# Performance work log

Hardware: AMD Instinct MI355X
Metric: run time of the kernel (lower is better)

## Reference

```python
import jax, jax.numpy as jnp
import numpy as np

N_NODES = 200000
E = 100000
H = 128            # hidden_dim = memory_dim = time_dim
EF = 64            # edge_feat_dim (raw_msg_dim)
L = 50             # price_seq_dim
LH = 32            # LSTM hidden size
MSG_DIM = EF + 2 * H + H  # IdentityMessage output = 448
N_PARTIES, N_STATES = 8, 56


def setup_inputs() -> dict:
    key = jax.random.key(0)
    ks = jax.random.split(key, 32)
    f = lambda k, shp, s=0.05: jax.random.normal(k, shp, dtype=jnp.float32) * s
    return {
        "src": jax.random.randint(ks[0], (E,), 0, N_NODES),
        "dst": jax.random.randint(ks[1], (E,), 0, N_NODES),
        "t": jnp.sort(jax.random.randint(ks[2], (E,), 0, 1000000)),
        "msg": jax.random.normal(ks[3], (E, EF), dtype=jnp.float32),
        "price_seq": jax.random.normal(ks[4], (E, L), dtype=jnp.float32),
        "trade_t": jax.random.randint(ks[5], (E,), 0, 1000000),
        "x_static": jax.random.randint(ks[6], (N_NODES, 2), 0, N_PARTIES),
        # TGN memory state
        "memory": f(ks[7], (N_NODES, H), 0.1),
        "last_update": jax.random.uniform(ks[8], (N_NODES,), dtype=jnp.float32) * 1000.0,
        # time encoder: cos(Linear(dt))
        "w_t": f(ks[9], (H,), 0.01),
        "b_t": f(ks[10], (H,)),
        # GRUCell memory updater
        "W_ih": f(ks[11], (3 * H, MSG_DIM)),
        "b_ih": f(ks[12], (3 * H,)),
        "W_hh": f(ks[13], (3 * H, H)),
        "b_hh": f(ks[14], (3 * H,)),
        # static embeddings + projection
        "party_emb": f(ks[15], (N_PARTIES, 16), 1.0),
        "state_emb": f(ks[16], (N_STATES, 16), 1.0),
        "W_sp": f(ks[17], (H, 32)),
        "b_sp": f(ks[18], (H,)),
        # price LSTM (input_size=1, hidden=32)
        "W_ih_l": f(ks[19], (4 * LH, 1)),
        "W_hh_l": f(ks[20], (4 * LH, LH)),
        "b_ih_l": f(ks[21], (4 * LH,)),
        "b_hh_l": f(ks[22], (4 * LH,)),
        "W_pp": f(ks[23], (H, LH)),
        "b_pp": f(ks[24], (H,)),
        # predictor MLP (dropout inactive at inference)
        "W1": f(ks[25], (64, 3 * H)),
        "b1": f(ks[26], (64,)),
        "W2": f(ks[27], (1, 64)),
        "b2": f(ks[28], (1,)),
    }


def reference(src, dst, t, msg, price_seq, trade_t, x_static, memory, last_update,
              w_t, b_t, W_ih, b_ih, W_hh, b_hh, party_emb, state_emb, W_sp, b_sp,
              W_ih_l, W_hh_l, b_ih_l, b_hh_l, W_pp, b_pp, W1, b1, W2, b2):
    N, Hd = memory.shape
    tf = t.astype(jnp.float32)
    t_enc = lambda dt: jnp.cos(dt[:, None] * w_t[None, :] + b_t[None, :])

    # ---- TGNMemory.update_state: gather -> message -> last-aggregate -> GRU scatter ----
    mem_s, mem_d = memory[src], memory[dst]
    msg_s = jnp.concatenate([mem_s, mem_d, msg, t_enc(tf - last_update[src])], axis=-1)
    msg_d = jnp.concatenate([mem_d, mem_s, msg, t_enc(tf - last_update[dst])], axis=-1)
    msgs = jnp.concatenate([msg_s, msg_d], axis=0)        # [2E, MSG_DIM]
    idx = jnp.concatenate([src, dst])                     # [2E]
    te = jnp.concatenate([tf, tf])
    M = idx.shape[0]
    # LastAggregator: per node, keep the message with the largest t (ties -> later event)
    perm = jnp.argsort(te)                                # stable ascending
    ranks = jnp.zeros((M,), jnp.int32).at[perm].set(jnp.arange(M, dtype=jnp.int32))
    win_rank = jax.ops.segment_max(ranks, idx, num_segments=N)  # int32 min for empty segs
    has_msg = win_rank >= 0
    win = perm[jnp.clip(win_rank, 0, M - 1)]
    agg = jnp.where(has_msg[:, None], msgs[win], 0.0)     # [N, MSG_DIM]
    # GRUCell update (applied only to nodes with messages)
    gi = agg @ W_ih.T + b_ih
    gh = memory @ W_hh.T + b_hh
    ir, iz, inn = jnp.split(gi, 3, axis=-1)
    hr, hz, hn = jnp.split(gh, 3, axis=-1)
    r = jax.nn.sigmoid(ir + hr)
    z = jax.nn.sigmoid(iz + hz)
    n = jnp.tanh(inn + r * hn)
    mem_new = jnp.where(has_msg[:, None], (1.0 - z) * n + z * memory, memory)

    # ---- static embeddings ----
    sf = jnp.concatenate([party_emb[x_static[src, 0]], state_emb[x_static[src, 1]]], axis=1)
    src_static = sf @ W_sp.T + b_sp

    # ---- price LSTM (input_size=1) ----
    B = price_seq.shape[0]
    nLH = W_hh_l.shape[1]
    bias = b_ih_l + b_hh_l

    def step(carry, x_t):
        h, c = carry
        g = x_t[:, None] * W_ih_l[:, 0][None, :] + h @ W_hh_l.T + bias
        i, fg, gg, o = jnp.split(g, 4, axis=-1)
        c = jax.nn.sigmoid(fg) * c + jax.nn.sigmoid(i) * jnp.tanh(gg)
        h = jax.nn.sigmoid(o) * jnp.tanh(c)
        return (h, c), None

    h0 = jnp.zeros((B, nLH), price_seq.dtype)
    (h_n, _), _ = jax.lax.scan(step, (h0, h0), price_seq.T)
    price_emb = h_n @ W_pp.T + b_pp

    # ---- fuse contexts + predictor MLP (dropout = identity at eval) ----
    combined = jnp.concatenate([mem_new[src] + src_static,
                                mem_new[dst] + price_emb,
                                price_emb], axis=1)
    h1 = jax.nn.relu(combined @ W1.T + b1)
    return (h1 @ W2.T + b2)[:, 0]
```

## Files before the change

kernel.cpp:

```cpp
#include <hip/hip_runtime.h>
#include <stdint.h>

#define NN    200000
#define NE    100000
#define HD    128
#define EFD   64
#define NG    384

typedef unsigned long long u64;
typedef short bf16x8 __attribute__((ext_vector_type(8)));
typedef float f32x4  __attribute__((ext_vector_type(4)));

#define OFF_KEY   ((size_t)0)
#define OFF_CNT   ((size_t)1600000)
#define OFF_LIST  ((size_t)1600256)
#define OFF_UV    ((size_t)2400256)
#define OFF_HN    ((size_t)104800256)
#define OFF_A     ((size_t)117600256)
#define OFF_B     ((size_t)117608448)
#define OFF_C0    ((size_t)117616640)
#define OFF_WBF   ((size_t)117616896)
#define WS_NEED   ((size_t)118092032)

#define W1OFF 221184
#define GRUB  3128
#define LSTB  782

__device__ __forceinline__ float frcp(float x){ return __builtin_amdgcn_rcpf(x); }
__device__ __forceinline__ float sigf(float x){ return frcp(1.f + __expf(-x)); }
__device__ __forceinline__ float tanhf_(float x){ return 1.f - 2.f*frcp(__expf(2.f*x) + 1.f); }
__device__ __forceinline__ float4 ld4(const float* p){ return *reinterpret_cast<const float4*>(p); }

__device__ __forceinline__ short f2bf(float f){
  unsigned u = __float_as_uint(f);
  u += 0x7fffu + ((u>>16)&1u);
  return (short)(u>>16);
}
__device__ __forceinline__ unsigned cvtpk(float lo, float hi){
  unsigned r;
  asm("v_cvt_pk_bf16_f32 %0, %1, %2" : "=v"(r) : "v"(lo), "v"(hi));
  return r;
}
__device__ __forceinline__ void gl16(const void* g, void* l) {
  __builtin_amdgcn_global_load_lds(
      (const __attribute__((address_space(1))) void*)g,
      (__attribute__((address_space(3))) void*)l, 16, 0, 0);
}

__global__ void k_scatter(const int* __restrict__ src, const int* __restrict__ dst,
                          const int* __restrict__ t, u64* __restrict__ key) {
  int e = blockIdx.x*256 + threadIdx.x;
  if (e >= NE) return;
  u64 tt = (u64)(unsigned)(t[e] + 1);
  atomicMax(&key[src[e]], (tt<<18) | (u64)(unsigned)e);
  atomicMax(&key[dst[e]], (tt<<18) | (1ULL<<17) | (u64)(unsigned)e);
}

__global__ void k_compact(const u64* __restrict__ key, int* __restrict__ list,
                          int* __restrict__ count) {
  int n = blockIdx.x*256 + threadIdx.x;
  if (n >= NN) return;
  if (key[n] != 0ULL) { int p = atomicAdd(count, 1); list[p] = n; }
}

__global__ void k_pre(const float* __restrict__ W1, const float* __restrict__ W_sp,
                      const float* __restrict__ W_pp, const float* __restrict__ b_sp,
                      const float* __restrict__ b_pp, const float* __restrict__ b1,
                      float* __restrict__ A, float* __restrict__ B, float* __restrict__ c0)
{
  int tid = blockIdx.x*256 + threadIdx.x;
  if (tid < 2048) {
    int o = tid >> 5, j = tid & 31;
    float s = 0.f;
    for (int k = 0; k < 128; ++k) s = fmaf(W1[o*NG + k], W_sp[k*32 + j], s);
    A[tid] = s;
  } else if (tid < 4096) {
    int q = tid - 2048;
    int o = q >> 5, j = q & 31;
    float s = 0.f;
    for (int k = 0; k < 128; ++k)
      s = fmaf(W1[o*NG + 128 + k] + W1[o*NG + 256 + k], W_pp[k*32 + j], s);
    B[q] = s;
  } else if (tid < 4160) {
    int o = tid - 4096;
    float s = b1[o];
    for (int k = 0; k < 128; ++k) {
      s = fmaf(W1[o*NG + k], b_sp[k], s);
      s = fmaf(W1[o*NG + 128 + k] + W1[o*NG + 256 + k], b_pp[k], s);
    }
    c0[o] = s;
  }
}

__global__ void k_prew(const float* __restrict__ W_ih, const float* __restrict__ W_hh,
                       const float* __restrict__ W1, short* __restrict__ Wbf)
{
  int idx = blockIdx.x*256 + threadIdx.x;
  if (idx < 9*384*8) {
    int s   = idx & 7;
    int n   = (idx >> 3) % 384;
    int ch9 = idx / (384*8);
    int k8  = s ^ (n & 7);
    int k   = ch9*64 + k8*8;
    short v[8];
    #pragma unroll
    for (int e = 0; e < 8; ++e) {
      int kk = k + e;
      float f = (kk < 448) ? W_ih[(size_t)n*448 + kk] : W_hh[(size_t)n*HD + (kk-448)];
      v[e] = f2bf(f);
    }
    *reinterpret_cast<bf16x8*>(Wbf + (size_t)ch9*24576 + n*64 + s*8) =
        *reinterpret_cast<bf16x8*>(v);
  } else if (idx < 9*384*8 + 128*16) {
    int idx2 = idx - 9*384*8;
    int s = idx2 & 15, r = idx2 >> 4;
    int k8 = s ^ (r & 15);
    int k = k8*8;
    short v[8];
    #pragma unroll
    for (int e = 0; e < 8; ++e) {
      int kk = k + e;
      float f = (r < 64) ? W1[(size_t)r*NG + kk] : W1[(size_t)(r-64)*NG + 128 + kk];
      v[e] = f2bf(f);
    }
    *reinterpret_cast<bf16x8*>(Wbf + W1OFF + r*128 + s*8) =
        *reinterpret_cast<bf16x8*>(v);
  }
}

__global__ __launch_bounds__(512, 2) void k_gl(
    const u64* __restrict__ key, const int* __restrict__ list, const int* __restrict__ count,
    const int* __restrict__ src, const int* __restrict__ dst, const int* __restrict__ t,
    const float* __restrict__ msg, const float* __restrict__ memory,
    const float* __restrict__ last_update,
    const float* __restrict__ w_t, const float* __restrict__ b_t,
    const short* __restrict__ Wbf, const float* __restrict__ b_ih,
    const float* __restrict__ b_hh, float* __restrict__ uv,
    const float* __restrict__ price, const float* __restrict__ W_ihl,
    const float* __restrict__ W_hhl, const float* __restrict__ b_ihl,
    const float* __restrict__ b_hhl, float* __restrict__ hn_out)
{
  __shared__ char lds[60416];
  int bid = blockIdx.x;
  int tid = threadIdx.x;
  int wid = tid >> 6, lane = tid & 63;
  int lr = lane & 15, lk = lane >> 4;

  if (bid >= LSTB) {
    int g = bid - LSTB;
    short* Wsb   = reinterpret_cast<short*>(lds);
    short* Xsb   = reinterpret_cast<short*>(lds + 49152);
    float* bias4 = reinterpret_cast<float*>(lds + 57344);
    int*   sn_self  = reinterpret_cast<int*>(lds + 59392);
    int*   sn_other = reinterpret_cast<int*>(lds + 59648);
    int*   sn_e     = reinterpret_cast<int*>(lds + 59904);
    float* sn_dt    = reinterpret_cast<float*>(lds + 60160);
    short* Mn2 = &Wsb[16384];

    int cnt = count[0];
    int base = g * 64;
    if (base >= cnt) return;

    if (tid < 64) {
      int idx = base + tid;
      int cl = idx < cnt ? idx : (cnt - 1);
      int n = list[cl];
      u64 k = key[n];
      int e   = (int)(k & 0x1FFFFULL);
      int isd = (int)((k >> 17) & 1ULL);
      sn_self[tid]  = n;
      sn_other[tid] = isd ? src[e] : dst[e];
      sn_e[tid]     = e;
      sn_dt[tid]    = (float)t[e] - last_update[n];
    }
    if (tid < 128) {
      int h = tid;
      bias4[h]       = b_ih[h]       + b_hh[h];
      bias4[128 + h] = b_ih[128 + h] + b_hh[128 + h];
      bias4[256 + h] = b_ih[256 + h];
      bias4[384 + h] = b_hh[256 + h];
    }
    __syncthreads();

    f32x4 aR[4], aZ[4], aNX[4], aNM[4];
    #pragma unroll
    for (int mt = 0; mt < 4; ++mt) { aR[mt] = (f32x4)0.f; aZ[mt] = (f32x4)0.f;
                                     aNX[mt] = (f32x4)0.f; aNM[mt] = (f32x4)0.f; }

    int node8 = tid >> 3, k8s = tid & 7;

    float4 xA0, xB0, xA1, xB1, xA2, xB2, xA3, xB3, xA4, xB4;
    {
      const float* pSelf  = memory + (size_t)sn_self[node8]*HD  + k8s*8;
      const float* pOther = memory + (size_t)sn_other[node8]*HD + k8s*8;
      const float* pMsg   = msg + (size_t)sn_e[node8]*EFD + k8s*8;
      xA0 = ld4(pSelf);       xB0 = ld4(pSelf+4);
      xA1 = ld4(pSelf+64);    xB1 = ld4(pSelf+68);
      xA2 = ld4(pOther);      xB2 = ld4(pOther+4);
      xA3 = ld4(pOther+64);   xB3 = ld4(pOther+68);
      xA4 = ld4(pMsg);        xB4 = ld4(pMsg+4);
    }

    constexpr int WCH[9] = {0, 7, 1, 8, 2, 3, 4, 5, 6};
    constexpr int XST[9] = {0,-1, 1,-1, 2, 3, 4,-2,-2};

    int hrow = wid*16 + lr;
    int swzH = (hrow & 7);

    #pragma unroll
    for (int p = 0; p < 9; ++p) {
      const int W = WCH[p];
      #pragma unroll
      for (int i = 0; i < 6; ++i) {
        int q = i*512 + tid;
        gl16(Wbf + (size_t)W*24576 + q*8, &Wsb[q*8]);
      }
      if (XST[p] >= 0) {
        float4 fa, fb;
        switch (XST[p]) {
          case 0: fa = xA0; fb = xB0; break;
          case 1: fa = xA1; fb = xB1; break;
          case 2: fa = xA2; fb = xB2; break;
          case 3: fa = xA3; fb = xB3; break;
          default: fa = xA4; fb = xB4; break;
        }
        short xs[8];
        xs[0]=f2bf(fa.x); xs[1]=f2bf(fa.y); xs[2]=f2bf(fa.z); xs[3]=f2bf(fa.w);
        xs[4]=f2bf(fb.x); xs[5]=f2bf(fb.y); xs[6]=f2bf(fb.z); xs[7]=f2bf(fb.w);
        *reinterpret_cast<bf16x8*>(&Xsb[node8*64 + ((k8s ^ (node8&7))<<3)]) =
            *reinterpret_cast<bf16x8*>(xs);
      } else if (XST[p] == -2) {
        int kk = (W == 6 ? 64 : 0) + k8s*8;
        float dt = sn_dt[node8];
        short xs[8];
        #pragma unroll
        for (int q = 0; q < 8; ++q) xs[q] = f2bf(cosf(fmaf(dt, w_t[kk+q], b_t[kk+q])));
        *reinterpret_cast<bf16x8*>(&Xsb[node8*64 + ((k8s ^ (node8&7))<<3)]) =
            *reinterpret_cast<bf16x8*>(xs);
      }
      __syncthreads();

      #pragma unroll
      for (int ks = 0; ks < 2; ++ks) {
        int k8 = ks*4 + lk;
        int so = (k8 ^ swzH) << 3;
        bf16x8 bR = *reinterpret_cast<const bf16x8*>(&Wsb[(size_t)hrow*64 + so]);
        bf16x8 bZ = *reinterpret_cast<const bf16x8*>(&Wsb[(size_t)(128+hrow)*64 + so]);
        bf16x8 bN = *reinterpret_cast<const bf16x8*>(&Wsb[(size_t)(256+hrow)*64 + so]);
        #pragma unroll
        for (int mt = 0; mt < 4; ++mt) {
          int anode = mt*16 + lr;
          bf16x8 a = *reinterpret_cast<const bf16x8*>(&Xsb[anode*64 + ((k8 ^ (anode&7))<<3)]);
          aR[mt] = __builtin_amdgcn_mfma_f32_16x16x32_bf16(a, bR, aR[mt], 0, 0, 0);
          aZ[mt] = __builtin_amdgcn_mfma_f32_16x16x32_bf16(a, bZ, aZ[mt], 0, 0, 0);
          if (W < 7) aNX[mt] = __builtin_amdgcn_mfma_f32_16x16x32_bf16(a, bN, aNX[mt], 0, 0, 0);
          else       aNM[mt] = __builtin_amdgcn_mfma_f32_16x16x32_bf16(a, bN, aNM[mt], 0, 0, 0);
        }
      }
      __syncthreads();
    }

    #pragma unroll
    for (int i = 0; i < 4; ++i) {
      int q = i*512 + tid;
      gl16(Wbf + W1OFF + q*8, &Wsb[q*8]);
    }

    {
      int h = hrow;
      int k8h = h >> 3, eh = h & 7;
      float br_ = bias4[h], bz_ = bias4[128+h], bnx_ = bias4[256+h], bnm_ = bias4[384+h];
      #pragma unroll
      for (int mt = 0; mt < 4; ++mt) {
        #pragma unroll
        for (int i = 0; i < 4; ++i) {
          int node = mt*16 + lk*4 + i;
          float r  = sigf(aR[mt][i] + br_);
          float z  = sigf(aZ[mt][i] + bz_);
          float nv = tanhf_(aNX[mt][i] + bnx_ + r*(aNM[mt][i] + bnm_));
          float m  = memory[(size_t)sn_self[node]*HD + h];
          Mn2[node*128 + ((k8h ^ (node&15))<<3) + eh] = f2bf((1.f - z)*nv + z*m);
        }
      }
    }
    __syncthreads();

    {
      int orow = wid*16 + lr;
      f32x4 acc2[4];
      #pragma unroll
      for (int mt = 0; mt < 4; ++mt) acc2[mt] = (f32x4)0.f;
      #pragma unroll
      for (int kf = 0; kf < 4; ++kf) {
        int k8 = kf*4 + lk;
        bf16x8 b = *reinterpret_cast<const bf16x8*>(&Wsb[orow*128 + ((k8 ^ (orow&15))<<3)]);
        #pragma unroll
        for (int mt = 0; mt < 4; ++mt) {
          int anode = mt*16 + lr;
          bf16x8 a = *reinterpret_cast<const bf16x8*>(&Mn2[anode*128 + ((k8 ^ (anode&15))<<3)]);
          acc2[mt] = __builtin_amdgcn_mfma_f32_16x16x32_bf16(a, b, acc2[mt], 0, 0, 0);
        }
      }
      #pragma unroll
      for (int mt = 0; mt < 4; ++mt) {
        #pragma unroll
        for (int i = 0; i < 4; ++i) {
          int node = mt*16 + lk*4 + i;
          if (base + node < cnt)
            uv[(size_t)sn_self[node]*128 + orow] = acc2[mt][i];
        }
      }
    }
  } else {
    int l = bid;
    short* Wb   = reinterpret_cast<short*>(lds);
    float* ps   = reinterpret_cast<float*>(lds + 8192);
    float* hbuf = reinterpret_cast<float*>(lds + 33792);

    {
      int base = tid * 8;
      #pragma unroll
      for (int q = 0; q < 4; ++q) {
        unsigned pk = cvtpk(W_hhl[base + q*2], W_hhl[base + q*2 + 1]);
        reinterpret_cast<unsigned*>(Wb)[tid*4 + q] = pk;
      }
    }
    int ebase = l * 128;
    int m = NE - ebase; if (m > 128) m = 128;
    for (int i = tid; i < 128*50; i += 512) {
      int r = i / 50, cidx = i % 50;
      int rr = r < m ? r : m - 1;
      ps[i] = price[(size_t)(ebase + rr)*50 + cidx];
    }
    __syncthreads();

    bf16x8 bw[8];
    float wih8[8], bias8[8];
    #pragma unroll
    for (int tI = 0; tI < 8; ++tI) {
      int row = tI*16 + lr;
      bw[tI] = *reinterpret_cast<const bf16x8*>(&Wb[row*32 + lk*8]);
      wih8[tI] = W_ihl[row];
      bias8[tI] = b_ihl[row] + b_hhl[row];
    }

    int we = wid * 16;
    float* hb = hbuf + wid*576;

    float c8[4][2];
    #pragma unroll
    for (int i = 0; i < 4; ++i) { c8[i][0] = 0.f; c8[i][1] = 0.f; }
    bf16x8 afrag = {0,0,0,0,0,0,0,0};

    #pragma unroll 1
    for (int s = 0; s < 50; ++s) {
      float xv[4];
      #pragma unroll
      for (int i = 0; i < 4; ++i) xv[i] = ps[(we + lk*4 + i)*50 + s];
      f32x4 acc[8];
      #pragma unroll
      for (int tI = 0; tI < 8; ++tI) {
        f32x4 ci;
        #pragma unroll
        for (int i = 0; i < 4; ++i) ci[i] = fmaf(xv[i], wih8[tI], bias8[tI]);
        acc[tI] = __builtin_amdgcn_mfma_f32_16x16x32_bf16(afrag, bw[tI], ci, 0, 0, 0);
      }
      #pragma unroll
      for (int i = 0; i < 4; ++i) {
        #pragma unroll
        for (int p = 0; p < 2; ++p) {
          float ei = __expf(-acc[0+p][i]);
          float ef = __expf(-acc[2+p][i]);
          float eg = __expf(2.f*acc[4+p][i]);
          float eo = __expf(-acc[6+p][i]);
          float di = 1.f + ei, df_ = 1.f + ef, dg = eg + 1.f, do_ = 1.f + eo;
          float m1 = di*df_, m2 = do_*dg;
          float R  = frcp(m1*m2);
          float ig = R*df_*m2;
          float fg = R*di*m2;
          float og = R*m1*dg;
          float gg = fmaf(-2.f, R*m1*do_, 1.f);
          c8[i][p] = fmaf(fg, c8[i][p], ig*gg);
          float th = 1.f - 2.f*frcp(__expf(2.f*c8[i][p]) + 1.f);
          hb[(lk*4 + i)*36 + p*16 + lr] = og*th;
        }
      }
      asm volatile("s_waitcnt lgkmcnt(0)" ::: "memory");
      float4 h0 = *reinterpret_cast<const float4*>(&hb[lr*36 + lk*8]);
      float4 h1 = *reinterpret_cast<const float4*>(&hb[lr*36 + lk*8 + 4]);
      unsigned pk_[4];
      pk_[0] = cvtpk(h0.x, h0.y);
      pk_[1] = cvtpk(h0.z, h0.w);
      pk_[2] = cvtpk(h1.x, h1.y);
      pk_[3] = cvtpk(h1.z, h1.w);
      afrag = *reinterpret_cast<bf16x8*>(pk_);
    }

    int e_g = ebase + we + lr;
    if (e_g < NE) {
      float4 h0 = *reinterpret_cast<const float4*>(&hb[lr*36 + lk*8]);
      float4 h1 = *reinterpret_cast<const float4*>(&hb[lr*36 + lk*8 + 4]);
      *reinterpret_cast<float4*>(hn_out + (size_t)e_g*32 + lk*8)     = h0;
      *reinterpret_cast<float4*>(hn_out + (size_t)e_g*32 + lk*8 + 4) = h1;
    }
  }
}

__global__ __launch_bounds__(256) void k_final(
    const int* __restrict__ src, const int* __restrict__ dst, const int* __restrict__ xst,
    const float* __restrict__ party, const float* __restrict__ state,
    const float* __restrict__ uv, const float* __restrict__ hn,
    const float* __restrict__ A, const float* __restrict__ B, const float* __restrict__ c0,
    const float* __restrict__ W2, const float* __restrict__ b2, float* __restrict__ out)
{
  __shared__ float As[2048], Bs[2048], c0s[64], W2s[64];
  int tid = threadIdx.x;
  for (int i = tid; i < 2048; i += 256) { As[i] = A[i]; Bs[i] = B[i]; }
  if (tid < 64) { c0s[tid] = c0[tid]; W2s[tid] = W2[tid]; }
  __syncthreads();
  int e = blockIdx.x*256 + tid;
  if (e >= NE) return;
  int s = src[e], d = dst[e];
  int p = xst[2*s], stt = xst[2*s + 1];
  float4 sf4[8], hv4[8];
  #pragma unroll
  for (int i = 0; i < 4; ++i) sf4[i]   = ld4(party + p*16 + i*4);
  #pragma unroll
  for (int i = 0; i < 4; ++i) sf4[4+i] = ld4(state + stt*16 + i*4);
  #pragma unroll
  for (int i = 0; i < 8; ++i) hv4[i] = ld4(hn + (size_t)e*32 + i*4);
  const float* urow = uv + (size_t)s*128;
  const float* vrow = uv + (size_t)d*128 + 64;
  float oacc = b2[0];
  #pragma unroll 4
  for (int o4 = 0; o4 < 16; ++o4) {
    float4 u4 = ld4(urow + o4*4);
    float4 v4 = ld4(vrow + o4*4);
    float4 cc = *reinterpret_cast<const float4*>(&c0s[o4*4]);
    float4 w2 = *reinterpret_cast<const float4*>(&W2s[o4*4]);
    float hh[4] = {u4.x+v4.x+cc.x, u4.y+v4.y+cc.y, u4.z+v4.z+cc.z, u4.w+v4.w+cc.w};
    #pragma unroll
    for (int oo = 0; oo < 4; ++oo) {
      int o = o4*4 + oo;
      float acc = hh[oo];
      #pragma unroll
      for (int j4 = 0; j4 < 8; ++j4) {
        float4 a = *reinterpret_cast<const float4*>(&As[o*32 + j4*4]);
        float4 b = *reinterpret_cast<const float4*>(&Bs[o*32 + j4*4]);
        float4 sfv = sf4[j4], hvv = hv4[j4];
        acc = fmaf(a.x,sfv.x, fmaf(a.y,sfv.y, fmaf(a.z,sfv.z, fmaf(a.w,sfv.w, acc))));
        acc = fmaf(b.x,hvv.x, fmaf(b.y,hvv.y, fmaf(b.z,hvv.z, fmaf(b.w,hvv.w, acc))));
      }
      float w2v = (oo==0) ? w2.x : (oo==1) ? w2.y : (oo==2) ? w2.z : w2.w;
      oacc = fmaf(w2v, fmaxf(acc, 0.f), oacc);
    }
  }
  out[e] = oacc;
}

extern "C" void kernel_launch(void* const* d_in, const int* in_sizes, int n_in,
                              void* d_out, int out_size, void* d_ws, size_t ws_size,
                              hipStream_t stream) {
  const int*   src   = (const int*)d_in[0];
  const int*   dst   = (const int*)d_in[1];
  const int*   t     = (const int*)d_in[2];
  const float* msg   = (const float*)d_in[3];
  const float* price = (const float*)d_in[4];
  const int*   xst   = (const int*)d_in[6];
  const float* memory= (const float*)d_in[7];
  const float* lu    = (const float*)d_in[8];
  const float* w_t   = (const float*)d_in[9];
  const float* b_t   = (const float*)d_in[10];
  const float* W_ih  = (const float*)d_in[11];
  const float* b_ih  = (const float*)d_in[12];
  const float* W_hh  = (const float*)d_in[13];
  const float* b_hh  = (const float*)d_in[14];
  const float* party = (const float*)d_in[15];
  const float* state = (const float*)d_in[16];
  const float* W_sp  = (const float*)d_in[17];
  const float* b_sp  = (const float*)d_in[18];
  const float* W_ihl = (const float*)d_in[19];
  const float* W_hhl = (const float*)d_in[20];
  const float* b_ihl = (const float*)d_in[21];
  const float* b_hhl = (const float*)d_in[22];
  const float* W_pp  = (const float*)d_in[23];
  const float* b_pp  = (const float*)d_in[24];
  const float* W1    = (const float*)d_in[25];
  const float* b1    = (const float*)d_in[26];
  const float* W2    = (const float*)d_in[27];
  const float* b2    = (const float*)d_in[28];
  float* out = (float*)d_out;

  if (ws_size < WS_NEED) {
    (void)hipMemsetAsync(d_out, 0, (size_t)out_size*4, stream);
    return;
  }

  char* ws = (char*)d_ws;
  u64*   key  = (u64*)(ws + OFF_KEY);
  int*   cnt  = (int*)(ws + OFF_CNT);
  int*   list = (int*)(ws + OFF_LIST);
  float* uv   = (float*)(ws + OFF_UV);
  float* hn   = (float*)(ws + OFF_HN);
  float* A    = (float*)(ws + OFF_A);
  float* B    = (float*)(ws + OFF_B);
  float* c0   = (float*)(ws + OFF_C0);
  short* Wbf  = (short*)(ws + OFF_WBF);

  (void)hipMemsetAsync(ws, 0, OFF_LIST, stream);
  k_scatter<<<(NE+255)/256, 256, 0, stream>>>(src, dst, t, key);
  k_compact<<<(NN+255)/256, 256, 0, stream>>>(key, list, cnt);
  k_pre<<<17, 256, 0, stream>>>(W1, W_sp, W_pp, b_sp, b_pp, b1, A, B, c0);
  k_prew<<<116, 256, 0, stream>>>(W_ih, W_hh, W1, Wbf);
  k_gl<<<LSTB + GRUB, 512, 0, stream>>>(key, list, cnt, src, dst, t, msg, memory, lu,
                                        w_t, b_t, Wbf, b_ih, b_hh, uv,
                                        price, W_ihl, W_hhl, b_ihl, b_hhl, hn);
  k_final<<<(NE+255)/256, 256, 0, stream>>>(src, dst, xst, party, state, uv, hn,
                                            A, B, c0, W2, b2, out);
}
```

Measured before the change: 443.8 us.

## Halve GRU K-chunk to 32 to shrink LDS and allow three blocks per CU

Splits the GRU weight streaming from 9 chunks of K=64 into 18 chunks of K=32, re-swizzling the bf16 weight prepack to match. The LDS footprint drops from about 60KB to about 52KB, and launch bounds are raised to 3 blocks per CU. Input gathers are moved inside the loop per chunk, so the up-front register-held x values are gone. The aim is higher occupancy, traded for twice as many barriers and more serialized gather latency per chunk.

```diff
diff --git a/kernel.cpp b/kernel.cpp
--- a/kernel.cpp
+++ b/kernel.cpp
@@ -25,6 +25,15 @@
 #define W1OFF 221184
 #define GRUB  3128
 #define LSTB  782
+
+#define AR_XSB   24576
+#define AR_MN2   32768
+#define AR_SNS   49152
+#define AR_SNO   49408
+#define AR_SNE   49664
+#define AR_SNDT  49920
+#define AR_BIAS  50176
+#define AR_SIZE  52736
 
 __device__ __forceinline__ float frcp(float x){ return __builtin_amdgcn_rcpf(x); }
 __device__ __forceinline__ float sigf(float x){ return frcp(1.f + __expf(-x)); }
@@ -96,12 +105,12 @@
                        const float* __restrict__ W1, short* __restrict__ Wbf)
 {
   int idx = blockIdx.x*256 + threadIdx.x;
-  if (idx < 9*384*8) {
-    int s   = idx & 7;
-    int n   = (idx >> 3) % 384;
-    int ch9 = idx / (384*8);
-    int k8  = s ^ (n & 7);
-    int k   = ch9*64 + k8*8;
+  if (idx < 18*384*4) {
+    int s  = idx & 3;
+    int n  = (idx >> 2) % 384;
+    int ch = idx / (384*4);
+    int k8 = s ^ (n & 3);
+    int k  = ch*32 + k8*8;
     short v[8];
     #pragma unroll
     for (int e = 0; e < 8; ++e) {
@@ -109,10 +118,10 @@
       float f = (kk < 448) ? W_ih[(size_t)n*448 + kk] : W_hh[(size_t)n*HD + (kk-448)];
       v[e] = f2bf(f);
     }
-    *reinterpret_cast<bf16x8*>(Wbf + (size_t)ch9*24576 + n*64 + s*8) =
+    *reinterpret_cast<bf16x8*>(Wbf + (size_t)ch*12288 + n*32 + s*8) =
         *reinterpret_cast<bf16x8*>(v);
-  } else if (idx < 9*384*8 + 128*16) {
-    int idx2 = idx - 9*384*8;
+  } else if (idx < 18*384*4 + 128*16) {
+    int idx2 = idx - 18*384*4;
     int s = idx2 & 15, r = idx2 >> 4;
     int k8 = s ^ (r & 15);
     int k = k8*8;
@@ -128,7 +137,7 @@
   }
 }
 
-__global__ __launch_bounds__(512, 2) void k_gl(
+__global__ __launch_bounds__(512, 3) void k_gl(
     const u64* __restrict__ key, const int* __restrict__ list, const int* __restrict__ count,
     const int* __restrict__ src, const int* __restrict__ dst, const int* __restrict__ t,
     const float* __restrict__ msg, const float* __restrict__ memory,
@@ -140,7 +149,7 @@
     const float* __restrict__ W_hhl, const float* __restrict__ b_ihl,
     const float* __restrict__ b_hhl, float* __restrict__ hn_out)
 {
-  __shared__ char lds[60416];
+  __shared__ __align__(16) char lds[AR_SIZE];
   int bid = blockIdx.x;
   int tid = threadIdx.x;
   int wid = tid >> 6, lane = tid & 63;
@@ -149,13 +158,13 @@
   if (bid >= LSTB) {
     int g = bid - LSTB;
     short* Wsb   = reinterpret_cast<short*>(lds);
-    short* Xsb   = reinterpret_cast<short*>(lds + 49152);
-    float* bias4 = reinterpret_cast<float*>(lds + 57344);
-    int*   sn_self  = reinterpret_cast<int*>(lds + 59392);
-    int*   sn_other = reinterpret_cast<int*>(lds + 59648);
-    int*   sn_e     = reinterpret_cast<int*>(lds + 59904);
-    float* sn_dt    = reinterpret_cast<float*>(lds + 60160);
-    short* Mn2 = &Wsb[16384];
+    short* Xsb   = reinterpret_cast<short*>(lds + AR_XSB);
+    short* Mn2   = reinterpret_cast<short*>(lds + AR_MN2);
+    int*   sn_self  = reinterpret_cast<int*>(lds + AR_SNS);
+    int*   sn_other = reinterpret_cast<int*>(lds + AR_SNO);
+    int*   sn_e     = reinterpret_cast<int*>(lds + AR_SNE);
+    float* sn_dt    = reinterpret_cast<float*>(lds + AR_SNDT);
+    float* bias4    = reinterpret_cast<float*>(lds + AR_BIAS);
 
     int cnt = count[0];
     int base = g * 64;
@@ -187,74 +196,64 @@
     for (int mt = 0; mt < 4; ++mt) { aR[mt] = (f32x4)0.f; aZ[mt] = (f32x4)0.f;
                                      aNX[mt] = (f32x4)0.f; aNM[mt] = (f32x4)0.f; }
 
-    int node8 = tid >> 3, k8s = tid & 7;
-
-    float4 xA0, xB0, xA1, xB1, xA2, xB2, xA3, xB3, xA4, xB4;
-    {
-      const float* pSelf  = memory + (size_t)sn_self[node8]*HD  + k8s*8;
-      const float* pOther = memory + (size_t)sn_other[node8]*HD + k8s*8;
-      const float* pMsg   = msg + (size_t)sn_e[node8]*EFD + k8s*8;
-      xA0 = ld4(pSelf);       xB0 = ld4(pSelf+4);
-      xA1 = ld4(pSelf+64);    xB1 = ld4(pSelf+68);
-      xA2 = ld4(pOther);      xB2 = ld4(pOther+4);
-      xA3 = ld4(pOther+64);   xB3 = ld4(pOther+68);
-      xA4 = ld4(pMsg);        xB4 = ld4(pMsg+4);
-    }
-
-    constexpr int WCH[9] = {0, 7, 1, 8, 2, 3, 4, 5, 6};
-    constexpr int XST[9] = {0,-1, 1,-1, 2, 3, 4,-2,-2};
+    int node4 = tid >> 2, k8s = tid & 3;
+
+    constexpr int WCH[18] = {0,14, 1,15, 2,16, 3,17, 4,5,6,7,8,9,10,11,12,13};
+    constexpr int XSTt[18] = {0,-1, 1,-1, 2,-1, 3,-1, 4,5,6,7,8,9,10,11,12,13};
 
     int hrow = wid*16 + lr;
-    int swzH = (hrow & 7);
-
-    #pragma unroll
-    for (int p = 0; p < 9; ++p) {
+    int swzH = (hrow & 3);
+
+    #pragma unroll
+    for (int p = 0; p < 18; ++p) {
       const int W = WCH[p];
       #pragma unroll
-      for (int i = 0; i < 6; ++i) {
+      for (int i = 0; i < 3; ++i) {
         int q = i*512 + tid;
-        gl16(Wbf + (size_t)W*24576 + q*8, &Wsb[q*8]);
-      }
-      if (XST[p] >= 0) {
-        float4 fa, fb;
-        switch (XST[p]) {
-          case 0: fa = xA0; fb = xB0; break;
-          case 1: fa = xA1; fb = xB1; break;
-          case 2: fa = xA2; fb = xB2; break;
-          case 3: fa = xA3; fb = xB3; break;
-          default: fa = xA4; fb = xB4; break;
+        gl16(Wbf + (size_t)W*12288 + q*8, &Wsb[q*8]);
+      }
+      int xc = XSTt[p];
+      if (xc >= 0 && tid < 256) {
+        float xf[8];
+        if (xc <= 3) {
+          const float* q = memory + (size_t)sn_self[node4]*HD + xc*32 + k8s*8;
+          float4 a = ld4(q), b = ld4(q+4);
+          xf[0]=a.x; xf[1]=a.y; xf[2]=a.z; xf[3]=a.w; xf[4]=b.x; xf[5]=b.y; xf[6]=b.z; xf[7]=b.w;
+        } else if (xc <= 7) {
+          const float* q = memory + (size_t)sn_other[node4]*HD + (xc-4)*32 + k8s*8;
+          float4 a = ld4(q), b = ld4(q+4);
+          xf[0]=a.x; xf[1]=a.y; xf[2]=a.z; xf[3]=a.w; xf[4]=b.x; xf[5]=b.y; xf[6]=b.z; xf[7]=b.w;
+        } else if (xc <= 9) {
+          const float* q = msg + (size_t)sn_e[node4]*EFD + (xc-8)*32 + k8s*8;
+          float4 a = ld4(q), b = ld4(q+4);
+          xf[0]=a.x; xf[1]=a.y; xf[2]=a.z; xf[3]=a.w; xf[4]=b.x; xf[5]=b.y; xf[6]=b.z; xf[7]=b.w;
+        } else {
+          int kk = (xc-10)*32 + k8s*8;
+          float dt = sn_dt[node4];
+          #pragma unroll
+          for (int q = 0; q < 8; ++q) xf[q] = cosf(fmaf(dt, w_t[kk+q], b_t[kk+q]));
         }
         short xs[8];
-        xs[0]=f2bf(fa.x); xs[1]=f2bf(fa.y); xs[2]=f2bf(fa.z); xs[3]=f2bf(fa.w);
-        xs[4]=f2bf(fb.x); xs[5]=f2bf(fb.y); xs[6]=f2bf(fb.z); xs[7]=f2bf(fb.w);
-        *reinterpret_cast<bf16x8*>(&Xsb[node8*64 + ((k8s ^ (node8&7))<<3)]) =
+        #pragma unroll
+        for (int q = 0; q < 8; ++q) xs[q] = f2bf(xf[q]);
+        *reinterpret_cast<bf16x8*>(&Xsb[node4*32 + ((k8s ^ (node4&3))<<3)]) =
             *reinterpret_cast<bf16x8*>(xs);
-      } else if (XST[p] == -2) {
-        int kk = (W == 6 ? 64 : 0) + k8s*8;
-        float dt = sn_dt[node8];
-        short xs[8];
-        #pragma unroll
-        for (int q = 0; q < 8; ++q) xs[q] = f2bf(cosf(fmaf(dt, w_t[kk+q], b_t[kk+q])));
-        *reinterpret_cast<bf16x8*>(&Xsb[node8*64 + ((k8s ^ (node8&7))<<3)]) =
-            *reinterpret_cast<bf16x8*>(xs);
       }
       __syncthreads();
 
-      #pragma unroll
-      for (int ks = 0; ks < 2; ++ks) {
-        int k8 = ks*4 + lk;
-        int so = (k8 ^ swzH) << 3;
-        bf16x8 bR = *reinterpret_cast<const bf16x8*>(&Wsb[(size_t)hrow*64 + so]);
-        bf16x8 bZ = *reinterpret_cast<const bf16x8*>(&Wsb[(size_t)(128+hrow)*64 + so]);
-        bf16x8 bN = *reinterpret_cast<const bf16x8*>(&Wsb[(size_t)(256+hrow)*64 + so]);
+      {
+        int so = (lk ^ swzH) << 3;
+        bf16x8 bR = *reinterpret_cast<const bf16x8*>(&Wsb[(size_t)hrow*32 + so]);
+        bf16x8 bZ = *reinterpret_cast<const bf16x8*>(&Wsb[(size_t)(128+hrow)*32 + so]);
+        bf16x8 bN = *reinterpret_cast<const bf16x8*>(&Wsb[(size_t)(256+hrow)*32 + so]);
         #pragma unroll
         for (int mt = 0; mt < 4; ++mt) {
           int anode = mt*16 + lr;
-          bf16x8 a = *reinterpret_cast<const bf16x8*>(&Xsb[anode*64 + ((k8 ^ (anode&7))<<3)]);
+          bf16x8 a = *reinterpret_cast<const bf16x8*>(&Xsb[anode*32 + ((lk ^ (anode&3))<<3)]);
           aR[mt] = __builtin_amdgcn_mfma_f32_16x16x32_bf16(a, bR, aR[mt], 0, 0, 0);
           aZ[mt] = __builtin_amdgcn_mfma_f32_16x16x32_bf16(a, bZ, aZ[mt], 0, 0, 0);
-          if (W < 7) aNX[mt] = __builtin_amdgcn_mfma_f32_16x16x32_bf16(a, bN, aNX[mt], 0, 0, 0);
-          else       aNM[mt] = __builtin_amdgcn_mfma_f32_16x16x32_bf16(a, bN, aNM[mt], 0, 0, 0);
+          if (W < 14) aNX[mt] = __builtin_amdgcn_mfma_f32_16x16x32_bf16(a, bN, aNX[mt], 0, 0, 0);
+          else        aNM[mt] = __builtin_amdgcn_mfma_f32_16x16x32_bf16(a, bN, aNM[mt], 0, 0, 0);
         }
       }
       __syncthreads();
```

After: 507.4 us. +14.3%, slower.
